# Optimization experiments

Hardware: AMD Instinct MI355X
Metric: run time of the kernel (lower is better)

Reference implementation:

```python
import jax, jax.numpy as jnp
import numpy as np

B, L, D, H, FF = 2, 2048, 2048, 16, 8192
DH = D // H
NEG = -1e9


def setup_inputs() -> dict:
    key = jax.random.key(0)
    ks = jax.random.split(key, 9)
    x = jax.random.normal(ks[0], (B, L, D), dtype=jnp.float32)
    # additive causal mask, broadcastable to [B, H, L, L]
    causal = jnp.triu(jnp.full((L, L), NEG, dtype=jnp.float32), k=1)
    mask = causal[None, None, :, :]
    s = 1.0 / np.sqrt(D)
    Wq = jax.random.normal(ks[1], (D, D), dtype=jnp.float32) * s
    Wk = jax.random.normal(ks[2], (D, D), dtype=jnp.float32) * s
    Wv = jax.random.normal(ks[3], (D, D), dtype=jnp.float32) * s
    Wo = jax.random.normal(ks[4], (D, D), dtype=jnp.float32) * s
    W_up = jax.random.normal(ks[5], (FF, D), dtype=jnp.float32) * s
    b_up = jnp.zeros((FF,), dtype=jnp.float32)
    W_down = jax.random.normal(ks[6], (D, FF), dtype=jnp.float32) * (1.0 / np.sqrt(FF))
    return {"x": x, "mask": mask, "Wq": Wq, "Wk": Wk, "Wv": Wv, "Wo": Wo,
            "W_up": W_up, "b_up": b_up, "W_down": W_down}


def reference(x, mask, Wq, Wk, Wv, Wo, W_up, b_up, W_down):
    b, l, d = x.shape
    # projections (torch Linear: y = x @ W.T); reshape to [B, H, L, DH]
    q = (x @ Wq.T).reshape(b, l, H, DH).transpose(0, 2, 1, 3)
    k = (x @ Wk.T).reshape(b, l, H, DH).transpose(0, 2, 1, 3)
    v = (x @ Wv.T).reshape(b, l, H, DH).transpose(0, 2, 1, 3)
    # NOTE: original module applies NO 1/sqrt(d_head) scaling
    scores = jnp.einsum('bhqd,bhkd->bhqk', q, k) + mask
    attn = jax.nn.softmax(scores, axis=-1)
    out = jnp.einsum('bhqk,bhkd->bhqd', attn, v)
    out = out.transpose(0, 2, 1, 3).reshape(b, l, d)
    x = x + out @ Wo.T
    h = jax.nn.relu(x @ W_up.T + b_up)
    return x + h @ W_down.T
```

## Files before the change

### kernel.cpp

```cpp
#include <hip/hip_runtime.h>
#include <stdint.h>

typedef _Float16 f16;
typedef __attribute__((ext_vector_type(8))) _Float16 f16x8;
typedef __attribute__((ext_vector_type(4))) _Float16 f16x4;
typedef __attribute__((ext_vector_type(2))) __fp16 fp16x2;
typedef __attribute__((ext_vector_type(4))) float f32x4;
typedef __attribute__((ext_vector_type(16))) float f32x16;
typedef __attribute__((ext_vector_type(4))) unsigned u32x4;

__device__ __forceinline__ void gload16(void* lds, const void* gc) {
  void* g = const_cast<void*>(gc);
  __builtin_amdgcn_global_load_lds((__attribute__((address_space(1))) void*)g,
                                   (__attribute__((address_space(3))) void*)lds,
                                   16, 0, 0);
}

__device__ __forceinline__ unsigned pkrtz(float a, float b) {
  union { fp16x2 h; unsigned u; } c;
  c.h = __builtin_amdgcn_cvt_pkrtz(a, b);
  return c.u;
}

__global__ __launch_bounds__(256) void k_cast(const float* __restrict__ in,
                                              f16* __restrict__ out, int n4) {
  int stride = gridDim.x * blockDim.x;
  for (int i = blockIdx.x * blockDim.x + threadIdx.x; i < n4; i += stride) {
    float4 v = ((const float4*)in)[i];
    f16x4 o;
    o[0] = (f16)v.x; o[1] = (f16)v.y; o[2] = (f16)v.z; o[3] = (f16)v.w;
    ((f16x4*)out)[i] = o;
  }
}

__global__ __launch_bounds__(256) void k_cast4(const float* __restrict__ s0, const float* __restrict__ s1,
                                               const float* __restrict__ s2, const float* __restrict__ s3,
                                               f16* __restrict__ d0, f16* __restrict__ d1,
                                               f16* __restrict__ d2, f16* __restrict__ d3, int n4) {
  const int which = blockIdx.y;
  const float* in = which == 0 ? s0 : which == 1 ? s1 : which == 2 ? s2 : s3;
  f16* out = which == 0 ? d0 : which == 1 ? d1 : which == 2 ? d2 : d3;
  int stride = gridDim.x * blockDim.x;
  for (int i = blockIdx.x * blockDim.x + threadIdx.x; i < n4; i += stride) {
    float4 v = ((const float4*)in)[i];
    f16x4 o;
    o[0] = (f16)v.x; o[1] = (f16)v.y; o[2] = (f16)v.z; o[3] = (f16)v.w;
    ((f16x4*)out)[i] = o;
  }
}

__global__ __launch_bounds__(256) void k_cast2w(const float* __restrict__ s0, const float* __restrict__ s1,
                                                f16* __restrict__ d0, f16* __restrict__ d1, int n4) {
  const int which = blockIdx.y;
  const float* in = which == 0 ? s0 : s1;
  f16* out = which == 0 ? d0 : d1;
  int stride = gridDim.x * blockDim.x;
  for (int i = blockIdx.x * blockDim.x + threadIdx.x; i < n4; i += stride) {
    float4 v = ((const float4*)in)[i];
    f16x4 o;
    o[0] = (f16)v.x; o[1] = (f16)v.y; o[2] = (f16)v.z; o[3] = (f16)v.w;
    ((f16x4*)out)[i] = o;
  }
}

__global__ __launch_bounds__(256) void k_transpose_v(const f16* __restrict__ vp,
                                                     f16* __restrict__ vt) {
  __shared__ __attribute__((aligned(16))) f16 tile[64][66];
  const int lt = blockIdx.x, dt = blockIdx.y, bh = blockIdx.z;
  const int t = threadIdx.x;
  const int r = t >> 3, c = 8 * (t & 7);
  const f16* src = vp + ((size_t)bh * 2048 + lt * 64) * 128 + dt * 64;
#pragma unroll
  for (int i = 0; i < 2; ++i) {
    union { f16x8 v; unsigned u[4]; } uu;
    uu.v = *(const f16x8*)&src[(size_t)(i * 32 + r) * 128 + c];
#pragma unroll
    for (int j = 0; j < 4; ++j)
      *(unsigned*)&tile[i * 32 + r][c + 2 * j] = uu.u[j];
  }
  __syncthreads();
  f16* dst = vt + ((size_t)bh * 128 + dt * 64) * 2048 + lt * 64;
#pragma unroll
  for (int i = 0; i < 2; ++i) {
    const int dr = i * 32 + r;
    f16x8 o;
#pragma unroll
    for (int e = 0; e < 8; ++e) o[e] = tile[c + e][dr];
    *(f16x8*)&dst[(size_t)dr * 2048 + c] = o;
  }
}

__global__ __launch_bounds__(256) void k_fuseout(const f16* __restrict__ x1b,
                                                 const float* __restrict__ p0,
                                                 const float* __restrict__ p1,
                                                 float* __restrict__ out, int n4) {
  int stride = gridDim.x * blockDim.x;
  for (int i = blockIdx.x * blockDim.x + threadIdx.x; i < n4; i += stride) {
    float4 a = ((const float4*)p0)[i];
    float4 b = ((const float4*)p1)[i];
    f16x4 xb = ((const f16x4*)x1b)[i];
    float4 o;
    o.x = (float)xb[0] + a.x + b.x;
    o.y = (float)xb[1] + a.y + b.y;
    o.z = (float)xb[2] + a.z + b.z;
    o.w = (float)xb[3] + a.w + b.w;
    ((float4*)out)[i] = o;
  }
}

template <int EPI, int SPLITOUT, int BK>
__global__ __launch_bounds__(256, 4) void gemm_nt(const f16* __restrict__ A,
                                                  const f16* __restrict__ B,
                                                  int Kit, int ld, int N,
                                                  const float* __restrict__ res,
                                                  const float* __restrict__ bias,
                                                  float* __restrict__ outf,
                                                  float* __restrict__ outf2,
                                                  f16* __restrict__ outb,
                                                  f16* __restrict__ outb_lo,
                                                  f16* __restrict__ outv) {
  constexpr int TSZ = 128 * BK;
  constexpr int CH  = 2048;
  constexpr int RPC = CH / BK;
  constexpr int NCH = 128 / RPC;
  constexpr int CW  = BK / 8;
  __shared__ __attribute__((aligned(16))) f16 As[TSZ];
  __shared__ __attribute__((aligned(16))) f16 Bs[TSZ];
  const int t = threadIdx.x;
  const int l = t & 63;
  const int w = t >> 6;
  const int wr = w >> 1, wc = w & 1;

  const int nwg = gridDim.x * gridDim.y;
  const int id = blockIdx.y * gridDim.x + blockIdx.x;
  const int sw = (id & 7) * (nwg >> 3) + (id >> 3);
  const int bn = sw % gridDim.x;
  const int bm = sw / gridDim.x;
  const int k0 = blockIdx.z * Kit;

  f32x4 acc[4][4] = {};

  const size_t aoff = (size_t)bm * 128 * ld + k0;
  const size_t boff = (size_t)bn * 128 * ld + k0;

  const int sr = t / CW;
  const int sc = 8 * (t % CW);
  const int lbase = w * 512;

  const int lr = l & 15, lq = l >> 4;
  const int nk = Kit / BK;
  for (int kt = 0; kt < nk; ++kt) {
    const size_t gbase = (size_t)kt * BK + (size_t)sr * ld + sc;
#pragma unroll
    for (int j = 0; j < NCH; ++j) {
      gload16(As + j * CH + lbase, A + aoff + (size_t)j * RPC * ld + gbase);
      gload16(Bs + j * CH + lbase, B + boff + (size_t)j * RPC * ld + gbase);
    }
    __syncthreads();
#pragma unroll
    for (int kk = 0; kk < BK / 32; ++kk) {
      f16x8 af[4], bfr[4];
#pragma unroll
      for (int m = 0; m < 4; ++m)
        af[m] = *(const f16x8*)&As[(wr * 64 + m * 16 + lr) * BK + kk * 32 + 8 * lq];
#pragma unroll
      for (int n = 0; n < 4; ++n)
        bfr[n] = *(const f16x8*)&Bs[(wc * 64 + n * 16 + lr) * BK + kk * 32 + 8 * lq];
#pragma unroll
      for (int m = 0; m < 4; ++m)
#pragma unroll
        for (int n = 0; n < 4; ++n)
          acc[m][n] = __builtin_amdgcn_mfma_f32_16x16x32_f16(af[m], bfr[n], acc[m][n], 0, 0, 0);
    }
    __syncthreads();
  }

  const size_t QKS = (size_t)8 << 20;
#pragma unroll
  for (int m = 0; m < 4; ++m) {
#pragma unroll
    for (int r = 0; r < 4; ++r) {
      const int grow = bm * 128 + wr * 64 + m * 16 + lq * 4 + r;
#pragma unroll
      for (int n = 0; n < 4; ++n) {
        const int gcol = bn * 128 + wc * 64 + n * 16 + lr;
        const float v = acc[m][n][r];
        if constexpr (EPI == 0) {
          const int which = gcol >> 11;
          const int hcol = gcol & 2047;
          const int bb = grow >> 11, ll = grow & 2047;
          const int hh = hcol >> 7, dh = hcol & 127;
          const size_t idx = ((size_t)((bb * 16 + hh) * 2048 + ll) << 7) + dh;
          const f16 hv = (f16)v;
          if (which == 2) {
            outv[idx] = hv;
          } else {
            outb[which * QKS + idx] = hv;
            if constexpr (SPLITOUT) outb_lo[which * QKS + idx] = (f16)(v - (float)hv);
          }
        } else if constexpr (EPI == 1) {
          const size_t idx = (size_t)grow * N + gcol;
          outb[idx] = (f16)(res[idx] + v);
        } else if constexpr (EPI == 2) {
          const size_t idx = (size_t)grow * N + gcol;
          outb[idx] = (f16)fmaxf(v + bias[gcol], 0.f);
        } else {
          const size_t idx = (size_t)grow * N + gcol;
          (blockIdx.z ? outf2 : outf)[idx] = v;
        }
      }
    }
  }
}

__global__ __launch_bounds__(256) void k_attn(const f16* __restrict__ q_hi,
                                              const f16* __restrict__ q_lo,
                                              const f16* __restrict__ k_hi,
                                              const f16* __restrict__ k_lo,
                                              const f16* __restrict__ vtp,
                                              f16* __restrict__ op) {
  __shared__ __attribute__((aligned(16))) f16 Ks_hi[64 * 128];
  __shared__ __attribute__((aligned(16))) f16 Ks_lo[64 * 128];
  __shared__ __attribute__((aligned(16))) f16 Vs[128 * 64];
  const int t = threadIdx.x, l = t & 63, w = t >> 6;
  const int flat = (int)blockIdx.x;
  const int s_ = flat >> 5;
  const int bh = flat & 31;
  const int qb = (s_ < 8) ? (15 - s_) : (s_ - 8);
  const int q0 = qb * 128;
  const int lh = l >> 5, lm = l & 31;
  const int wrow0 = q0 + 32 * w;
  const int myrow = wrow0 + lm;

  const f16* qhp = q_hi + (size_t)bh * 2048 * 128;
  const f16* qlp = q_lo + (size_t)bh * 2048 * 128;
  const f16* khp = k_hi + (size_t)bh * 2048 * 128;
  const f16* klp = k_lo + (size_t)bh * 2048 * 128;
  const f16* vhp = vtp + (size_t)bh * 128 * 2048;

  const int krow = t >> 4, kg = t & 15;
  const int vrow = t >> 3, vg = t & 7;

  f16x8 aqh[8], aql[8];
#pragma unroll
  for (int c = 0; c < 8; ++c) {
    const size_t qi = (size_t)myrow * 128 + c * 16 + 8 * lh;
    aqh[c] = *(const f16x8*)&qhp[qi];
    aql[c] = *(const f16x8*)&qlp[qi];
  }

  f32x16 acc[4] = {};
  float mr = -1e30f, sr = 0.f;

  const int ntile = 2 * qb + 2;
  for (int kt = 0; kt < ntile; ++kt) {
    f16x8 tkh[4], tkl[4], tv[4];
#pragma unroll
    for (int i = 0; i < 4; ++i) {
      const size_t ki = (size_t)(kt * 64 + i * 16 + krow) * 128 + 8 * kg;
      tkh[i] = *(const f16x8*)&khp[ki];
      tkl[i] = *(const f16x8*)&klp[ki];
      tv[i] = *(const f16x8*)&vhp[(size_t)(i * 32 + vrow) * 2048 + kt * 64 + 8 * vg];
    }
    __syncthreads();
#pragma unroll
    for (int i = 0; i < 4; ++i) {
      const int kr = i * 16 + krow;
      const int g = kg ^ (kr & 7);
      *(f16x8*)&Ks_hi[kr * 128 + 8 * g] = tkh[i];
      *(f16x8*)&Ks_lo[kr * 128 + 8 * g] = tkl[i];
      const int vr = i * 32 + vrow;
      const int gv = vg ^ (vr & 7);
      *(f16x8*)&Vs[vr * 64 + 8 * gv] = tv[i];
    }
    __syncthreads();

    if (kt * 64 >= wrow0 + 32) continue;

    f32x16 s0, s1;
    __builtin_amdgcn_s_setprio(1);
    {
      f32x16 zh = {}, zl = {};
#pragma unroll
      for (int c = 0; c < 8; ++c) {
        const int g = (2 * c + lh) ^ (lm & 7);
        const f16x8 bh_ = *(const f16x8*)&Ks_hi[lm * 128 + 8 * g];
        const f16x8 bl_ = *(const f16x8*)&Ks_lo[lm * 128 + 8 * g];
        zh = __builtin_amdgcn_mfma_f32_32x32x16_f16(bh_, aqh[c], zh, 0, 0, 0);
        zl = __builtin_amdgcn_mfma_f32_32x32x16_f16(bh_, aql[c], zl, 0, 0, 0);
        zl = __builtin_amdgcn_mfma_f32_32x32x16_f16(bl_, aqh[c], zl, 0, 0, 0);
      }
      s0 = zh + zl;
    }
    {
      f32x16 zh = {}, zl = {};
#pragma unroll
      for (int c = 0; c < 8; ++c) {
        const int g = (2 * c + lh) ^ (lm & 7);
        const f16x8 bh_ = *(const f16x8*)&Ks_hi[(32 + lm) * 128 + 8 * g];
        const f16x8 bl_ = *(const f16x8*)&Ks_lo[(32 + lm) * 128 + 8 * g];
        zh = __builtin_amdgcn_mfma_f32_32x32x16_f16(bh_, aqh[c], zh, 0, 0, 0);
        zl = __builtin_amdgcn_mfma_f32_32x32x16_f16(bh_, aql[c], zl, 0, 0, 0);
        zl = __builtin_amdgcn_mfma_f32_32x32x16_f16(bl_, aqh[c], zl, 0, 0, 0);
      }
      s1 = zh + zl;
    }
    __builtin_amdgcn_s_setprio(0);

    if (kt * 64 + 63 > wrow0) {
#pragma unroll
      for (int j = 0; j < 16; ++j) {
        const int keyl = (j & 3) + 8 * (j >> 2) + 4 * lh;
        if (kt * 64 + keyl > myrow) s0[j] = -1e30f;
        if (kt * 64 + 32 + keyl > myrow) s1[j] = -1e30f;
      }
    }

    float m = -1e30f;
#pragma unroll
    for (int j = 0; j < 16; ++j) m = fmaxf(m, fmaxf(s0[j], s1[j]));
    m = fmaxf(m, __shfl_xor(m, 32));
    if (__any(m > mr + 8.f)) {
      const float mnew = fmaxf(mr, m);
      const float sc = __expf(mr - mnew);
      mr = mnew;
      sr *= sc;
#pragma unroll
      for (int j = 0; j < 16; ++j) {
        const float scj = __shfl(sc, (j & 3) + 8 * (j >> 2) + 4 * lh + 32 * (l >> 5 ? 0 : 0));
#pragma unroll
        for (int ct = 0; ct < 4; ++ct) acc[ct][j] *= scj;
      }
    }
    float p0v[16], p1v[16];
    float ts = 0.f;
#pragma unroll
    for (int j = 0; j < 16; ++j) {
      p0v[j] = __expf(s0[j] - mr);
      p1v[j] = __expf(s1[j] - mr);
      ts += p0v[j] + p1v[j];
    }
    sr += ts + __shfl_xor(ts, 32);

    unsigned u[16];
#pragma unroll
    for (int m2 = 0; m2 < 8; ++m2) {
      u[m2] = pkrtz(p0v[2 * m2], p0v[2 * m2 + 1]);
      u[8 + m2] = pkrtz(p1v[2 * m2], p1v[2 * m2 + 1]);
    }
    unsigned ys[8];
#pragma unroll
    for (int m2 = 0; m2 < 8; ++m2) {
      const int q_ = m2 >> 1, h_ = m2 & 1;
      const unsigned xs = lh ? u[4 * q_ + h_] : u[4 * q_ + 2 + h_];
      ys[m2] = __shfl_xor(xs, 32);
    }
    f16x8 pf[4];
#pragma unroll
    for (int kk = 0; kk < 4; ++kk) {
      union { u32x4 u4; f16x8 h8; } cv;
      if (lh == 0) {
        cv.u4[0] = u[4 * kk];     cv.u4[1] = u[4 * kk + 1];
        cv.u4[2] = ys[2 * kk];    cv.u4[3] = ys[2 * kk + 1];
      } else {
        cv.u4[0] = ys[2 * kk];    cv.u4[1] = ys[2 * kk + 1];
        cv.u4[2] = u[4 * kk + 2]; cv.u4[3] = u[4 * kk + 3];
      }
      pf[kk] = cv.h8;
    }

    __builtin_amdgcn_s_setprio(1);
#pragma unroll
    for (int ct = 0; ct < 4; ++ct) {
      const int dcol = ct * 32 + lm;
#pragma unroll
      for (int kk = 0; kk < 4; ++kk) {
        const int gv = (2 * kk + lh) ^ (dcol & 7);
        const f16x8 bv = *(const f16x8*)&Vs[dcol * 64 + 8 * gv];
        acc[ct] = __builtin_amdgcn_mfma_f32_32x32x16_f16(pf[kk], bv, acc[ct], 0, 0, 0);
      }
    }
    __builtin_amdgcn_s_setprio(0);
  }

  const int bb = bh >> 4, hh = bh & 15;
  const float inv = 1.f / sr;
#pragma unroll
  for (int j = 0; j < 16; ++j) {
    const int rl = (j & 3) + 8 * (j >> 2) + 4 * lh;
    const float invj = __shfl(inv, rl);
    const size_t row = (size_t)(bb * 2048 + wrow0 + rl);
#pragma unroll
    for (int ct = 0; ct < 4; ++ct)
      op[row * 2048 + hh * 128 + ct * 32 + lm] = (f16)(acc[ct][j] * invj);
  }
}

extern "C" void kernel_launch(void* const* d_in, const int* in_sizes, int n_in,
                              void* d_out, int out_size, void* d_ws, size_t ws_size,
                              hipStream_t stream) {
  const float* x   = (const float*)d_in[0];
  const float* Wq  = (const float*)d_in[2];
  const float* Wk  = (const float*)d_in[3];
  const float* Wv  = (const float*)d_in[4];
  const float* Wo  = (const float*)d_in[5];
  const float* Wup = (const float*)d_in[6];
  const float* bup = (const float*)d_in[7];
  const float* Wdn = (const float*)d_in[8];
  float* out = (float*)d_out;

  const size_t M1 = 1u << 20;
  f16* W = (f16*)d_ws;
  f16* x_hi    = W + 0 * M1;
  f16* wqkv_hi = W + 8 * M1;
  f16* wo_hi   = W + 20 * M1;
  f16* wup_hi  = W + 24 * M1;
  f16* wdn_hi  = W + 40 * M1;
  f16* q_hi    = W + 56 * M1;
  f16* q_lo    = W + 72 * M1;
  f16* vp      = W + 88 * M1;
  f16* vtb     = W + 96 * M1;
  f16* x1b   = x_hi;
  float* p0  = (float*)(W + 24 * M1);
  f16* hb    = W + 56 * M1;
  float* p1  = (float*)(W + 88 * M1);
  f16* attno = vp;
  if (ws_size < (size_t)104 * M1 * sizeof(f16)) return;

  auto cg = [](size_t n4) { size_t g = (n4 + 255) / 256; return (unsigned)(g > 2048 ? 2048 : g); };
  dim3 b256(256);
  k_cast<<<cg(2 * M1), b256, 0, stream>>>(x, x_hi, (int)(2 * M1));
  k_cast4<<<dim3(cg(1 * M1), 4), b256, 0, stream>>>(
      Wq, Wk, Wv, Wo,
      wqkv_hi, wqkv_hi + 4 * M1, wqkv_hi + 8 * M1, wo_hi, (int)(1 * M1));
  k_cast2w<<<dim3(cg(4 * M1), 2), b256, 0, stream>>>(
      Wup, Wdn, wup_hi, wdn_hi, (int)(4 * M1));

  gemm_nt<0, 1, 64><<<dim3(48, 32), b256, 0, stream>>>(
      x_hi, wqkv_hi, 2048, 2048, 6144,
      nullptr, nullptr, nullptr, nullptr, q_hi, q_lo, vp);
  k_transpose_v<<<dim3(32, 2, 32), b256, 0, stream>>>(vp, vtb);
  k_attn<<<dim3(512), b256, 0, stream>>>(
      q_hi, q_lo, q_hi + 8 * M1, q_lo + 8 * M1, vtb, attno);
  gemm_nt<1, 0, 64><<<dim3(16, 32), b256, 0, stream>>>(
      attno, wo_hi, 2048, 2048, 2048,
      x, nullptr, nullptr, nullptr, x1b, nullptr, nullptr);
  gemm_nt<2, 0, 64><<<dim3(64, 32), b256, 0, stream>>>(
      x1b, wup_hi, 2048, 2048, 8192,
      nullptr, bup, nullptr, nullptr, hb, nullptr, nullptr);
  gemm_nt<3, 0, 64><<<dim3(16, 32, 2), b256, 0, stream>>>(
      hb, wdn_hi, 4096, 8192, 2048,
      nullptr, nullptr, p0, p1, nullptr, nullptr, nullptr);
  k_fuseout<<<2048, b256, 0, stream>>>(x1b, p0, p1, out, (int)(2 * M1));
}
```

Before: 752.7 us.

## Add 256x256 double-buffered 8-wave GEMM for QKV, up and down projections

Introduces a new gemm8 kernel with 512 threads, a 256x256 output tile, double-buffered LDS staging with an XOR swizzle, explicit waitcnt/barrier scheduling, and setprio around the MFMA blocks. It is used for the QKV, up and down projections, while the old kernel is kept only for the Wo projection with its residual epilogue. The larger tile is meant to raise data reuse per global load and to overlap the next tile's loads with compute. The cost is more LDS and register pressure, fewer workgroups (wave quantization on the smaller grids), and reliance on hand-placed vmcnt counts being correct.

```diff
diff --git a/kernel.cpp b/kernel.cpp
--- a/kernel.cpp
+++ b/kernel.cpp
@@ -113,12 +113,7 @@
                                                   const f16* __restrict__ B,
                                                   int Kit, int ld, int N,
                                                   const float* __restrict__ res,
-                                                  const float* __restrict__ bias,
-                                                  float* __restrict__ outf,
-                                                  float* __restrict__ outf2,
-                                                  f16* __restrict__ outb,
-                                                  f16* __restrict__ outb_lo,
-                                                  f16* __restrict__ outv) {
+                                                  f16* __restrict__ outb) {
   constexpr int TSZ = 128 * BK;
   constexpr int CH  = 2048;
   constexpr int RPC = CH / BK;
@@ -136,12 +131,11 @@
   const int sw = (id & 7) * (nwg >> 3) + (id >> 3);
   const int bn = sw % gridDim.x;
   const int bm = sw / gridDim.x;
-  const int k0 = blockIdx.z * Kit;
 
   f32x4 acc[4][4] = {};
 
-  const size_t aoff = (size_t)bm * 128 * ld + k0;
-  const size_t boff = (size_t)bn * 128 * ld + k0;
+  const size_t aoff = (size_t)bm * 128 * ld;
+  const size_t boff = (size_t)bn * 128 * ld;
 
   const int sr = t / CW;
   const int sc = 8 * (t % CW);
@@ -175,7 +169,6 @@
     __syncthreads();
   }
 
-  const size_t QKS = (size_t)8 << 20;
 #pragma unroll
   for (int m = 0; m < 4; ++m) {
 #pragma unroll
@@ -184,6 +177,146 @@
 #pragma unroll
       for (int n = 0; n < 4; ++n) {
         const int gcol = bn * 128 + wc * 64 + n * 16 + lr;
+        const size_t idx = (size_t)grow * N + gcol;
+        outb[idx] = (f16)(res[idx] + acc[m][n][r]);
+      }
+    }
+  }
+}
+
+template <int EPI, int SPLITOUT>
+__global__ __launch_bounds__(512, 2) void gemm8(const f16* __restrict__ A,
+                                                const f16* __restrict__ B,
+                                                int Kit, int ld, int N,
+                                                const float* __restrict__ bias,
+                                                float* __restrict__ outf,
+                                                float* __restrict__ outf2,
+                                                f16* __restrict__ outb,
+                                                f16* __restrict__ outb_lo,
+                                                f16* __restrict__ outv) {
+  __shared__ __attribute__((aligned(16))) f16 As[2 * 16384];
+  __shared__ __attribute__((aligned(16))) f16 Bs[2 * 16384];
+  const int t = threadIdx.x;
+  const int l = t & 63;
+  const int w = t >> 6;
+  const int wm = w >> 2, wn = w & 3;
+
+  const int nwg = gridDim.x * gridDim.y;
+  const int id = blockIdx.y * gridDim.x + blockIdx.x;
+  const int sw = (id & 7) * (nwg >> 3) + (id >> 3);
+  const int bn = sw % gridDim.x;
+  const int bm = sw / gridDim.x;
+  const int k0 = blockIdx.z * Kit;
+
+  const size_t aoff = (size_t)(bm * 256) * ld + k0;
+  const size_t boff = (size_t)(bn * 256) * ld + k0;
+
+  const int rstage = t >> 3;
+  const int gstage = (t & 7) ^ ((t >> 3) & 7);
+  const int ldsb = (t >> 6) * 512;
+
+  auto stage = [&](int tt, int b) {
+    const size_t col = (size_t)tt * 64 + gstage * 8;
+#pragma unroll
+    for (int j = 0; j < 4; ++j) {
+      const size_t grow = (size_t)(j * 64 + rstage) * ld + col;
+      gload16(As + b * 16384 + j * 4096 + ldsb, A + aoff + grow);
+      gload16(Bs + b * 16384 + j * 4096 + ldsb, B + boff + grow);
+    }
+  };
+
+  f32x4 acc[8][4] = {};
+
+  const int lr = l & 15, lq = l >> 4;
+  const int x7 = lr & 7;
+  const int nt = Kit >> 6;
+
+  stage(0, 0);
+  stage(1, 1);
+  asm volatile("s_waitcnt vmcnt(8)" ::: "memory");
+  __builtin_amdgcn_s_barrier();
+
+  for (int kt = 0; kt < nt; ++kt) {
+    const int b = kt & 1;
+    const f16* Ab = As + b * 16384;
+    const f16* Bb = Bs + b * 16384;
+    f16x8 af[4][2], bf[4][2];
+#pragma unroll
+    for (int m = 0; m < 4; ++m)
+#pragma unroll
+      for (int ks = 0; ks < 2; ++ks)
+        af[m][ks] = *(const f16x8*)&Ab[((wm * 128 + m * 16 + lr) * 8 + ((ks * 4 + lq) ^ x7)) * 8];
+#pragma unroll
+    for (int n = 0; n < 4; ++n)
+#pragma unroll
+      for (int ks = 0; ks < 2; ++ks)
+        bf[n][ks] = *(const f16x8*)&Bb[((wn * 64 + n * 16 + lr) * 8 + ((ks * 4 + lq) ^ x7)) * 8];
+    __builtin_amdgcn_s_barrier();
+    __builtin_amdgcn_s_setprio(1);
+#pragma unroll
+    for (int m = 0; m < 4; ++m)
+#pragma unroll
+      for (int n = 0; n < 2; ++n)
+#pragma unroll
+        for (int ks = 0; ks < 2; ++ks)
+          acc[m][n] = __builtin_amdgcn_mfma_f32_16x16x32_f16(af[m][ks], bf[n][ks], acc[m][n], 0, 0, 0);
+    __builtin_amdgcn_s_setprio(0);
+    __builtin_amdgcn_s_barrier();
+    __builtin_amdgcn_s_setprio(1);
+#pragma unroll
+    for (int m = 0; m < 4; ++m)
+#pragma unroll
+      for (int n = 2; n < 4; ++n)
+#pragma unroll
+        for (int ks = 0; ks < 2; ++ks)
+          acc[m][n] = __builtin_amdgcn_mfma_f32_16x16x32_f16(af[m][ks], bf[n][ks], acc[m][n], 0, 0, 0);
+    __builtin_amdgcn_s_setprio(0);
+    __builtin_amdgcn_s_barrier();
+#pragma unroll
+    for (int m = 0; m < 4; ++m)
+#pragma unroll
+      for (int ks = 0; ks < 2; ++ks)
+        af[m][ks] = *(const f16x8*)&Ab[((wm * 128 + 64 + m * 16 + lr) * 8 + ((ks * 4 + lq) ^ x7)) * 8];
+    asm volatile("s_waitcnt lgkmcnt(0)" ::: "memory");
+    __builtin_amdgcn_sched_barrier(0);
+    __builtin_amdgcn_s_barrier();
+    if (kt + 2 < nt) stage(kt + 2, b);
+    __builtin_amdgcn_s_setprio(1);
+#pragma unroll
+    for (int m = 0; m < 4; ++m)
+#pragma unroll
+      for (int n = 0; n < 2; ++n)
+#pragma unroll
+        for (int ks = 0; ks < 2; ++ks)
+          acc[4 + m][n] = __builtin_amdgcn_mfma_f32_16x16x32_f16(af[m][ks], bf[n][ks], acc[4 + m][n], 0, 0, 0);
+    __builtin_amdgcn_s_setprio(0);
+    __builtin_amdgcn_s_barrier();
+    __builtin_amdgcn_s_setprio(1);
+#pragma unroll
+    for (int m = 0; m < 4; ++m)
+#pragma unroll
+      for (int n = 2; n < 4; ++n)
+#pragma unroll
+        for (int ks = 0; ks < 2; ++ks)
+          acc[4 + m][n] = __builtin_amdgcn_mfma_f32_16x16x32_f16(af[m][ks], bf[n][ks], acc[4 + m][n], 0, 0, 0);
+    __builtin_amdgcn_s_setprio(0);
+    if (kt + 2 < nt) {
+      asm volatile("s_waitcnt vmcnt(8)" ::: "memory");
+    } else {
+      asm volatile("s_waitcnt vmcnt(0)" ::: "memory");
+    }
+    __builtin_amdgcn_s_barrier();
+  }
+
+  const size_t QKS = (size_t)8 << 20;
+#pragma unroll
+  for (int m = 0; m < 8; ++m) {
+#pragma unroll
+    for (int r = 0; r < 4; ++r) {
+      const int grow = bm * 256 + wm * 128 + m * 16 + lq * 4 + r;
+#pragma unroll
+      for (int n = 0; n < 4; ++n) {
+        const int gcol = bn * 256 + wn * 64 + n * 16 + lr;
         const float v = acc[m][n][r];
         if constexpr (EPI == 0) {
           const int which = gcol >> 11;
@@ -198,9 +331,6 @@
             outb[which * QKS + idx] = hv;
             if constexpr (SPLITOUT) outb_lo[which * QKS + idx] = (f16)(v - (float)hv);
           }
-        } else if constexpr (EPI == 1) {
-          const size_t idx = (size_t)grow * N + gcol;
-          outb[idx] = (f16)(res[idx] + v);
         } else if constexpr (EPI == 2) {
           const size_t idx = (size_t)grow * N + gcol;
           outb[idx] = (f16)fmaxf(v + bias[gcol], 0.f);
@@ -327,7 +457,7 @@
       sr *= sc;
 #pragma unroll
       for (int j = 0; j < 16; ++j) {
-        const float scj = __shfl(sc, (j & 3) + 8 * (j >> 2) + 4 * lh + 32 * (l >> 5 ? 0 : 0));
+        const float scj = __shfl(sc, (j & 3) + 8 * (j >> 2) + 4 * lh);
 #pragma unroll
         for (int ct = 0; ct < 4; ++ct) acc[ct][j] *= scj;
       }
@@ -429,6 +559,7 @@
 
   auto cg = [](size_t n4) { size_t g = (n4 + 255) / 256; return (unsigned)(g > 2048 ? 2048 : g); };
   dim3 b256(256);
+  dim3 b512(512);
   k_cast<<<cg(2 * M1), b256, 0, stream>>>(x, x_hi, (int)(2 * M1));
   k_cast4<<<dim3(cg(1 * M1), 4), b256, 0, stream>>>(
       Wq, Wk, Wv, Wo,
@@ -436,20 +567,19 @@
   k_cast2w<<<dim3(cg(4 * M1), 2), b256, 0, stream>>>(
       Wup, Wdn, wup_hi, wdn_hi, (int)(4 * M1));
 
-  gemm_nt<0, 1, 64><<<dim3(48, 32), b256, 0, stream>>>(
+  gemm8<0, 1><<<dim3(24, 16), b512, 0, stream>>>(
       x_hi, wqkv_hi, 2048, 2048, 6144,
-      nullptr, nullptr, nullptr, nullptr, q_hi, q_lo, vp);
+      nullptr, nullptr, nullptr, q_hi, q_lo, vp);
   k_transpose_v<<<dim3(32, 2, 32), b256, 0, stream>>>(vp, vtb);
   k_attn<<<dim3(512), b256, 0, stream>>>(
       q_hi, q_lo, q_hi + 8 * M1, q_lo + 8 * M1, vtb, attno);
   gemm_nt<1, 0, 64><<<dim3(16, 32), b256, 0, stream>>>(
-      attno, wo_hi, 2048, 2048, 2048,
-      x, nullptr, nullptr, nullptr, x1b, nullptr, nullptr);
-  gemm_nt<2, 0, 64><<<dim3(64, 32), b256, 0, stream>>>(
+      attno, wo_hi, 2048, 2048, 2048, x, x1b);
+  gemm8<2, 0><<<dim3(32, 16), b512, 0, stream>>>(
       x1b, wup_hi, 2048, 2048, 8192,
-      nullptr, bup, nullptr, nullptr, hb, nullptr, nullptr);
-  gemm_nt<3, 0, 64><<<dim3(16, 32, 2), b256, 0, stream>>>(
+      bup, nullptr, nullptr, hb, nullptr, nullptr);
+  gemm8<3, 0><<<dim3(8, 16, 2), b512, 0, stream>>>(
       hb, wdn_hi, 4096, 8192, 2048,
-      nullptr, nullptr, p0, p1, nullptr, nullptr, nullptr);
+      nullptr, p0, p1, nullptr, nullptr, nullptr);
   k_fuseout<<<2048, b256, 0, stream>>>(x1b, p0, p1, out, (int)(2 * M1));
 }
```

New measurement: 722.9 us. 1.04x faster.
